# Kernel tuning notes

Measured on AMD Instinct MI355X. Metric: run time of the kernel, lower is better.

Reference implementation:

```python
import jax, jax.numpy as jnp
import numpy as np

N = 100000  # nodes per type (user, tweet)
E = 500000  # edges per relation
D = 128     # input feature dim
H = 128     # hidden dim


def _seg_mean(h_src, src, dst, n_dst):
    # DGL copy_u + mean: mean of source features over incoming edges; zero for in-degree 0.
    msg = h_src[src]                                                    # [E, F] gather
    s = jax.ops.segment_sum(msg, dst, num_segments=n_dst)               # [n_dst, F] scatter-add
    cnt = jax.ops.segment_sum(jnp.ones((src.shape[0], 1), h_src.dtype), dst, num_segments=n_dst)
    return s / jnp.maximum(cnt, 1.0)


def setup_inputs() -> dict:
    key = jax.random.key(0)
    ks = jax.random.split(key, 24)
    f = lambda i, shp, s=1.0: jax.random.normal(ks[i], shp, dtype=jnp.float32) * s
    return {
        'x_user': f(0, (N, D)), 'x_tweet': f(1, (N, D)),
        # layer 1, relation 'posts' (user -> tweet) and 'posted_by' (tweet -> user)
        'w1ps': f(2, (H, D), 0.05), 'b1ps': f(3, (H,), 0.05),
        'w1pn': f(4, (H, D), 0.05), 'b1pn': f(5, (H,), 0.05),
        'w1bs': f(6, (H, D), 0.05), 'b1bs': f(7, (H,), 0.05),
        'w1bn': f(8, (H, D), 0.05), 'b1bn': f(9, (H,), 0.05),
        # layer 2 (out_feats = 1, no activation)
        'w2ps': f(10, (1, H), 0.05), 'b2ps': f(11, (1,), 0.05),
        'w2pn': f(12, (1, H), 0.05), 'b2pn': f(13, (1,), 0.05),
        'w2bs': f(14, (1, H), 0.05), 'b2bs': f(15, (1,), 0.05),
        'w2bn': f(16, (1, H), 0.05), 'b2bn': f(17, (1,), 0.05),
        'src_posts': jax.random.randint(ks[18], (E,), 0, N),
        'dst_posts': jax.random.randint(ks[19], (E,), 0, N),
        'src_pb': jax.random.randint(ks[20], (E,), 0, N),
        'dst_pb': jax.random.randint(ks[21], (E,), 0, N),
    }


def reference(x_user, x_tweet,
              w1ps, b1ps, w1pn, b1pn, w1bs, b1bs, w1bn, b1bn,
              w2ps, b2ps, w2pn, b2pn, w2bs, b2bs, w2bn, b2bn,
              src_posts, dst_posts, src_pb, dst_pb):
    # ---- conv1: DivFeatConv per relation, relu, cross-relation sum (one rel per dst type) ----
    neigh_t = _seg_mean(x_user, src_posts, dst_posts, N)               # user -posts-> tweet
    h_tweet = jax.nn.relu(x_tweet @ w1ps.T + b1ps + neigh_t @ w1pn.T + b1pn)
    neigh_u = _seg_mean(x_tweet, src_pb, dst_pb, N)                    # tweet -posted_by-> user
    h_user = jax.nn.relu(x_user @ w1bs.T + b1bs + neigh_u @ w1bn.T + b1bn)
    # ---- conv2: out_feats=1, identity activation ----
    neigh_t2 = _seg_mean(h_user, src_posts, dst_posts, N)
    out_tweet = h_tweet @ w2ps.T + b2ps + neigh_t2 @ w2pn.T + b2pn     # [N, 1]
    neigh_u2 = _seg_mean(h_tweet, src_pb, dst_pb, N)
    out_user = h_user @ w2bs.T + b2bs + neigh_u2 @ w2bn.T + b2bn       # [N, 1]
    return (out_user, out_tweet)
```

## Files before the change

kernel.cpp:

```cpp
#include <hip/hip_runtime.h>

#define N_NODES 100000
#define N_EDGES 500000
#define DIM 128
#define HSTR 4

typedef __attribute__((ext_vector_type(8))) short short8;
typedef __attribute__((ext_vector_type(4))) float f32x4;

__device__ __forceinline__ ushort f2bf(float f) {
    unsigned u = __float_as_uint(f);
    u += 0x7FFF + ((u >> 16) & 1);
    return (ushort)(u >> 16);
}
__device__ __forceinline__ float bf2f(ushort s) {
    return __uint_as_float(((unsigned)s) << 16);
}


__global__ __launch_bounds__(256) void build_lists2_kernel(
    const int* __restrict__ s0, const int* __restrict__ d0,
    const int* __restrict__ s1, const int* __restrict__ d1,
    int* __restrict__ head2, int2* __restrict__ entry2) {
    const int rel = blockIdx.y;
    const int* src = rel ? s1 : s0;
    const int* dst = rel ? d1 : d0;
    int* head = head2 + (size_t)rel * N_NODES * HSTR;
    int2* entry = entry2 + (size_t)rel * N_EDGES;
    int e = blockIdx.x * 256 + threadIdx.x;
    if (e < N_EDGES) {
        int d = dst[e];
        int old = atomicExch(&head[(size_t)d * HSTR], e);
        entry[e] = make_int2(src[e], old);
    }
}


__global__ __launch_bounds__(256) void cvtw_kernel(
    const float* __restrict__ w0, const float* __restrict__ w1,
    const float* __restrict__ w2, const float* __restrict__ w3,
    ushort* __restrict__ o0, ushort* __restrict__ o1,
    ushort* __restrict__ o2, ushort* __restrict__ o3) {
    int a = blockIdx.y;
    const float* in = (a == 0) ? w0 : (a == 1) ? w1 : (a == 2) ? w2 : w3;
    ushort* out = (a == 0) ? o0 : (a == 1) ? o1 : (a == 2) ? o2 : o3;
    int i = (blockIdx.x * 256 + threadIdx.x) * 4;
    float4 v = *reinterpret_cast<const float4*>(&in[i]);
    ushort4 u = make_ushort4(f2bf(v.x), f2bf(v.y), f2bf(v.z), f2bf(v.w));
    *reinterpret_cast<ushort4*>(&out[i]) = u;
}

__global__ __launch_bounds__(256) void cvtx_kernel(const float* __restrict__ x0,
                                                   const float* __restrict__ x1,
                                                   ushort* __restrict__ o0,
                                                   ushort* __restrict__ o1) {
    const float* in = blockIdx.y ? x1 : x0;
    ushort* out = blockIdx.y ? o1 : o0;
    int i = (blockIdx.x * 256 + threadIdx.x) * 4;
    float4 v = *reinterpret_cast<const float4*>(&in[i]);
    ushort4 u = make_ushort4(f2bf(v.x), f2bf(v.y), f2bf(v.z), f2bf(v.w));
    *reinterpret_cast<ushort4*>(&out[i]) = u;
}


__global__ __launch_bounds__(256) void seg_mean_bf16_list_kernel(
    const ushort* __restrict__ x, const int* __restrict__ head,
    const int2* __restrict__ entry, ushort* __restrict__ outbf) {
    int idx = blockIdx.x * 256 + threadIdx.x;
    int node = idx >> 4;
    if (node >= N_NODES) return;
    int f = (idx & 15) << 3;
    float acc[8];
#pragma unroll
    for (int j = 0; j < 8; ++j) acc[j] = 0.f;
    int cnt = 0;
    int e = head[(size_t)node * HSTR];
    while (e >= 0) {
        int2 nd = entry[e];
        ++cnt;
        short8 v = *reinterpret_cast<const short8*>(&x[(size_t)nd.x * DIM + f]);
#pragma unroll
        for (int j = 0; j < 8; ++j) acc[j] += bf2f((ushort)v[j]);
        e = nd.y;
    }
    float r = 1.0f / fmaxf((float)cnt, 1.0f);
    union { ushort s[8]; uint4 v; } u;
#pragma unroll
    for (int j = 0; j < 8; ++j) u.s[j] = f2bf(acc[j] * r);
    *reinterpret_cast<uint4*>(&outbf[(size_t)node * DIM + f]) = u.v;
}

__global__ __launch_bounds__(256) void seg_mean_f32_list_kernel(
    const float* __restrict__ x, const int* __restrict__ head,
    const int2* __restrict__ entry, ushort* __restrict__ outbf) {
    int idx = blockIdx.x * 256 + threadIdx.x;
    int node = idx >> 5;
    if (node >= N_NODES) return;
    int f = (idx & 31) << 2;
    float4 acc = make_float4(0.f, 0.f, 0.f, 0.f);
    int cnt = 0;
    int e = head[(size_t)node * HSTR];
    while (e >= 0) {
        int2 nd = entry[e];
        ++cnt;
        float4 v = *reinterpret_cast<const float4*>(&x[(size_t)nd.x * DIM + f]);
        acc.x += v.x; acc.y += v.y; acc.z += v.z; acc.w += v.w;
        e = nd.y;
    }
    float r = 1.0f / fmaxf((float)cnt, 1.0f);
    ushort4 u = make_ushort4(f2bf(acc.x * r), f2bf(acc.y * r),
                             f2bf(acc.z * r), f2bf(acc.w * r));
    *reinterpret_cast<ushort4*>(&outbf[node * DIM + f]) = u;
}

__global__ __launch_bounds__(256) void gemm_mfma_bf_kernel(
    const ushort* __restrict__ Xsbf,
    const ushort* __restrict__ Nm,
    const ushort* __restrict__ Wsbf,
    const ushort* __restrict__ Wnbf,
    const float* __restrict__ bs, const float* __restrict__ bn,
    const float* __restrict__ w2a, const float* __restrict__ w2b,
    float* __restrict__ dself, float* __restrict__ dcross) {
    __shared__ ushort sA[128 * 64];
    __shared__ ushort sB[128 * 64];
    __shared__ float pS[2][2][128];

    const int tid = threadIdx.x;
    const int lane = tid & 63;
    const int wid = tid >> 6;
    const int wr = wid >> 1, wc = wid & 1;
    const int lr = lane & 15, lg = lane >> 4;
    const int row0 = blockIdx.x * 128;

    f32x4 acc[4][4];
#pragma unroll
    for (int i = 0; i < 4; ++i)
#pragma unroll
        for (int j = 0; j < 4; ++j) acc[i][j] = (f32x4){0.f, 0.f, 0.f, 0.f};

    const int r = tid >> 1;
    const int hh = tid & 1;
    const int grow = row0 + r;
    const int swzr = (r & 7) << 4;

    for (int kb = 0; kb < 256; kb += 64) {
        const int kg = kb & 127;
        const bool self = (kb < 128);
        __syncthreads();
        {
            const uint4* g = reinterpret_cast<const uint4*>(self ? Xsbf : Nm);
#pragma unroll
            for (int q = 0; q < 4; ++q) {
                uint4 v = make_uint4(0, 0, 0, 0);
                if (grow < N_NODES)
                    v = g[((size_t)grow * DIM + kg + hh * 32 + q * 8) >> 3];
                int byte = (hh * 64 + q * 16) ^ swzr;
                *reinterpret_cast<uint4*>(&sA[r * 64 + (byte >> 1)]) = v;
            }
        }
        {
            const uint4* g = reinterpret_cast<const uint4*>(self ? Wsbf : Wnbf);
#pragma unroll
            for (int q = 0; q < 4; ++q) {
                uint4 v = g[(r * DIM + kg + hh * 32 + q * 8) >> 3];
                int byte = (hh * 64 + q * 16) ^ swzr;
                *reinterpret_cast<uint4*>(&sB[r * 64 + (byte >> 1)]) = v;
            }
        }
        __syncthreads();
#pragma unroll
        for (int ks = 0; ks < 2; ++ks) {
            short8 a[4], b[4];
#pragma unroll
            for (int fm = 0; fm < 4; ++fm) {
                int rr = wr * 64 + fm * 16 + lr;
                int byte = (ks * 64 + lg * 16) ^ ((rr & 7) << 4);
                a[fm] = *reinterpret_cast<const short8*>(&sA[rr * 64 + (byte >> 1)]);
            }
#pragma unroll
            for (int fn = 0; fn < 4; ++fn) {
                int cc = wc * 64 + fn * 16 + lr;
                int byte = (ks * 64 + lg * 16) ^ ((cc & 7) << 4);
                b[fn] = *reinterpret_cast<const short8*>(&sB[cc * 64 + (byte >> 1)]);
            }
#pragma unroll
            for (int fm = 0; fm < 4; ++fm)
#pragma unroll
                for (int fn = 0; fn < 4; ++fn)
                    acc[fm][fn] = __builtin_amdgcn_mfma_f32_16x16x32_bf16(
                        a[fm], b[fn], acc[fm][fn], 0, 0, 0);
        }
    }

    float bias[4], wa[4], wb[4];
#pragma unroll
    for (int fn = 0; fn < 4; ++fn) {
        int c = wc * 64 + fn * 16 + lr;
        bias[fn] = bs[c] + bn[c];
        wa[fn] = w2a[c];
        wb[fn] = w2b[c];
    }
#pragma unroll
    for (int fm = 0; fm < 4; ++fm) {
#pragma unroll
        for (int reg = 0; reg < 4; ++reg) {
            float pa = 0.f, pb = 0.f;
#pragma unroll
            for (int fn = 0; fn < 4; ++fn) {
                float h = fmaxf(acc[fm][fn][reg] + bias[fn], 0.f);
                pa = fmaf(h, wa[fn], pa);
                pb = fmaf(h, wb[fn], pb);
            }
#pragma unroll
            for (int m = 1; m < 16; m <<= 1) {
                pa += __shfl_xor(pa, m);
                pb += __shfl_xor(pb, m);
            }
            if (lr == 0) {
                int rloc = wr * 64 + fm * 16 + lg * 4 + reg;
                pS[wc][0][rloc] = pa;
                pS[wc][1][rloc] = pb;
            }
        }
    }
    __syncthreads();
    if (tid < 128) {
        int go = row0 + tid;
        if (go < N_NODES) {
            dself[go] = pS[0][0][tid] + pS[1][0][tid];
            dcross[go] = pS[0][1][tid] + pS[1][1][tid];
        }
    }
}

__global__ __launch_bounds__(256) void gemm_mfma_kernel(
    const float* __restrict__ Xs, const ushort* __restrict__ Nm,
    const ushort* __restrict__ Wsbf, const ushort* __restrict__ Wnbf,
    const float* __restrict__ bs, const float* __restrict__ bn,
    const float* __restrict__ w2a, const float* __restrict__ w2b,
    float* __restrict__ dself, float* __restrict__ dcross) {
    __shared__ ushort sA[128 * 64];
    __shared__ ushort sB[128 * 64];
    __shared__ float pS[2][2][128];

    const int tid = threadIdx.x;
    const int lane = tid & 63;
    const int wid = tid >> 6;
    const int wr = wid >> 1, wc = wid & 1;
    const int lr = lane & 15, lg = lane >> 4;
    const int row0 = blockIdx.x * 128;

    f32x4 acc[4][4];
#pragma unroll
    for (int i = 0; i < 4; ++i)
#pragma unroll
        for (int j = 0; j < 4; ++j) acc[i][j] = (f32x4){0.f, 0.f, 0.f, 0.f};

    const int r = tid >> 1;
    const int hh = tid & 1;
    const int grow = row0 + r;
    const int swzr = (r & 7) << 4;

    for (int kb = 0; kb < 256; kb += 64) {
        const int kg = kb & 127;
        const bool self = (kb < 128);
        __syncthreads();
        if (self) {
            const float4* g = reinterpret_cast<const float4*>(Xs);
#pragma unroll
            for (int q = 0; q < 4; ++q) {
                float4 v0 = make_float4(0.f, 0.f, 0.f, 0.f), v1 = v0;
                if (grow < N_NODES) {
                    size_t bi = ((size_t)grow * DIM + kg + hh * 32 + q * 8) >> 2;
                    v0 = g[bi];
                    v1 = g[bi + 1];
                }
                union { ushort s[8]; uint4 v; } u;
                u.s[0] = f2bf(v0.x); u.s[1] = f2bf(v0.y);
                u.s[2] = f2bf(v0.z); u.s[3] = f2bf(v0.w);
                u.s[4] = f2bf(v1.x); u.s[5] = f2bf(v1.y);
                u.s[6] = f2bf(v1.z); u.s[7] = f2bf(v1.w);
                int byte = (hh * 64 + q * 16) ^ swzr;
                *reinterpret_cast<uint4*>(&sA[r * 64 + (byte >> 1)]) = u.v;
            }
        } else {
            const uint4* g = reinterpret_cast<const uint4*>(Nm);
#pragma unroll
            for (int q = 0; q < 4; ++q) {
                uint4 v = make_uint4(0, 0, 0, 0);
                if (grow < N_NODES)
                    v = g[((size_t)grow * DIM + kg + hh * 32 + q * 8) >> 3];
                int byte = (hh * 64 + q * 16) ^ swzr;
                *reinterpret_cast<uint4*>(&sA[r * 64 + (byte >> 1)]) = v;
            }
        }
        {
            const uint4* g = reinterpret_cast<const uint4*>(self ? Wsbf : Wnbf);
#pragma unroll
            for (int q = 0; q < 4; ++q) {
                uint4 v = g[(r * DIM + kg + hh * 32 + q * 8) >> 3];
                int byte = (hh * 64 + q * 16) ^ swzr;
                *reinterpret_cast<uint4*>(&sB[r * 64 + (byte >> 1)]) = v;
            }
        }
        __syncthreads();
#pragma unroll
        for (int ks = 0; ks < 2; ++ks) {
            short8 a[4], b[4];
#pragma unroll
            for (int fm = 0; fm < 4; ++fm) {
                int rr = wr * 64 + fm * 16 + lr;
                int byte = (ks * 64 + lg * 16) ^ ((rr & 7) << 4);
                a[fm] = *reinterpret_cast<const short8*>(&sA[rr * 64 + (byte >> 1)]);
            }
#pragma unroll
            for (int fn = 0; fn < 4; ++fn) {
                int cc = wc * 64 + fn * 16 + lr;
                int byte = (ks * 64 + lg * 16) ^ ((cc & 7) << 4);
                b[fn] = *reinterpret_cast<const short8*>(&sB[cc * 64 + (byte >> 1)]);
            }
#pragma unroll
            for (int fm = 0; fm < 4; ++fm)
#pragma unroll
                for (int fn = 0; fn < 4; ++fn)
                    acc[fm][fn] = __builtin_amdgcn_mfma_f32_16x16x32_bf16(
                        a[fm], b[fn], acc[fm][fn], 0, 0, 0);
        }
    }

    float bias[4], wa[4], wb[4];
#pragma unroll
    for (int fn = 0; fn < 4; ++fn) {
        int c = wc * 64 + fn * 16 + lr;
        bias[fn] = bs[c] + bn[c];
        wa[fn] = w2a[c];
        wb[fn] = w2b[c];
    }
#pragma unroll
    for (int fm = 0; fm < 4; ++fm) {
#pragma unroll
        for (int reg = 0; reg < 4; ++reg) {
            float pa = 0.f, pb = 0.f;
#pragma unroll
            for (int fn = 0; fn < 4; ++fn) {
                float h = fmaxf(acc[fm][fn][reg] + bias[fn], 0.f);
                pa = fmaf(h, wa[fn], pa);
                pb = fmaf(h, wb[fn], pb);
            }
#pragma unroll
            for (int m = 1; m < 16; m <<= 1) {
                pa += __shfl_xor(pa, m);
                pb += __shfl_xor(pb, m);
            }
            if (lr == 0) {
                int rloc = wr * 64 + fm * 16 + lg * 4 + reg;
                pS[wc][0][rloc] = pa;
                pS[wc][1][rloc] = pb;
            }
        }
    }
    __syncthreads();
    if (tid < 128) {
        int go = row0 + tid;
        if (go < N_NODES) {
            dself[go] = pS[0][0][tid] + pS[1][0][tid];
            dcross[go] = pS[0][1][tid] + pS[1][1][tid];
        }
    }
}

__global__ __launch_bounds__(256) void scalar_finalize_kernel(
    const float* __restrict__ dself_u, const float* __restrict__ dself_t,
    const float* __restrict__ scross_u, const float* __restrict__ scross_t,
    const int* __restrict__ head2, const int2* __restrict__ entry2,
    const float* __restrict__ b2bs, const float* __restrict__ b2bn,
    const float* __restrict__ b2ps, const float* __restrict__ b2pn,
    float* __restrict__ out) {
    int i = blockIdx.x * 256 + threadIdx.x;
    if (i >= N_NODES) return;
    {
        float a = 0.f; int cnt = 0;
        int e = head2[(size_t)i * HSTR];
        while (e >= 0) {
            int2 nd = entry2[e];
            ++cnt;
            a += scross_u[nd.x];
            e = nd.y;
        }
        out[N_NODES + i] = dself_t[i] + a / fmaxf((float)cnt, 1.0f) + b2ps[0] + b2pn[0];
    }
    {
        float a = 0.f; int cnt = 0;
        int e = head2[((size_t)N_NODES + i) * HSTR];
        while (e >= 0) {
            int2 nd = entry2[(size_t)N_EDGES + e];
            ++cnt;
            a += scross_t[nd.x];
            e = nd.y;
        }
        out[i] = dself_u[i] + a / fmaxf((float)cnt, 1.0f) + b2bs[0] + b2bn[0];
    }
}

extern "C" void kernel_launch(void* const* d_in, const int* in_sizes, int n_in,
                              void* d_out, int out_size, void* d_ws, size_t ws_size,
                              hipStream_t stream) {
    const float* x_user  = (const float*)d_in[0];
    const float* x_tweet = (const float*)d_in[1];
    const float* w1ps = (const float*)d_in[2];  const float* b1ps = (const float*)d_in[3];
    const float* w1pn = (const float*)d_in[4];  const float* b1pn = (const float*)d_in[5];
    const float* w1bs = (const float*)d_in[6];  const float* b1bs = (const float*)d_in[7];
    const float* w1bn = (const float*)d_in[8];  const float* b1bn = (const float*)d_in[9];
    const float* w2ps = (const float*)d_in[10]; const float* b2ps = (const float*)d_in[11];
    const float* w2pn = (const float*)d_in[12]; const float* b2pn = (const float*)d_in[13];
    const float* w2bs = (const float*)d_in[14]; const float* b2bs = (const float*)d_in[15];
    const float* w2bn = (const float*)d_in[16]; const float* b2bn = (const float*)d_in[17];
    const int* src_posts = (const int*)d_in[18];
    const int* dst_posts = (const int*)d_in[19];
    const int* src_pb    = (const int*)d_in[20];
    const int* dst_pb    = (const int*)d_in[21];
    float* out = (float*)d_out;

    char* wsb = (char*)d_ws;
    ushort* nbf     = (ushort*)wsb;   wsb += (size_t)N_NODES * DIM * 2;
    int* head2      = (int*)wsb;      wsb += (size_t)2 * N_NODES * HSTR * 4;
    int2* entry2    = (int2*)wsb;     wsb += (size_t)2 * N_EDGES * 8;
    ushort* wbf_ps  = (ushort*)wsb;   wsb += (size_t)DIM * DIM * 2;
    ushort* wbf_pn  = (ushort*)wsb;   wsb += (size_t)DIM * DIM * 2;
    ushort* wbf_bs  = (ushort*)wsb;   wsb += (size_t)DIM * DIM * 2;
    ushort* wbf_bn  = (ushort*)wsb;   wsb += (size_t)DIM * DIM * 2;
    float* dself_t  = (float*)wsb;    wsb += (size_t)N_NODES * 4;
    float* scross_t = (float*)wsb;    wsb += (size_t)N_NODES * 4;
    float* dself_u  = (float*)wsb;    wsb += (size_t)N_NODES * 4;
    float* scross_u = (float*)wsb;    wsb += (size_t)N_NODES * 4;
    ushort* xbf_u   = (ushort*)wsb;   wsb += (size_t)N_NODES * DIM * 2;
    ushort* xbf_t   = (ushort*)wsb;   wsb += (size_t)N_NODES * DIM * 2;
    const bool use_bf = ((size_t)(wsb - (char*)d_ws) <= ws_size);

    const int* head_posts = head2;
    const int* head_pb    = head2 + (size_t)N_NODES * HSTR;
    const int2* ent_posts = entry2;
    const int2* ent_pb    = entry2 + N_EDGES;

    const int gE = (N_EDGES + 255) / 256;
    const int gN = (N_NODES + 255) / 256;
    const int gG = (N_NODES + 127) / 128;

    cvtw_kernel<<<dim3(16, 4), 256, 0, stream>>>(w1ps, w1pn, w1bs, w1bn,
                                                 wbf_ps, wbf_pn, wbf_bs, wbf_bn);
    if (use_bf)
        cvtx_kernel<<<dim3(12500, 2), 256, 0, stream>>>(x_user, x_tweet, xbf_u, xbf_t);

    hipMemsetAsync(head2, 0xFF, (size_t)2 * N_NODES * HSTR * sizeof(int), stream);
    build_lists2_kernel<<<dim3(gE, 2), 256, 0, stream>>>(src_posts, dst_posts,
                                                         src_pb, dst_pb, head2, entry2);

    if (use_bf) {
        seg_mean_bf16_list_kernel<<<(N_NODES * 16 + 255) / 256, 256, 0, stream>>>(
            xbf_u, head_posts, ent_posts, nbf);
        gemm_mfma_bf_kernel<<<gG, 256, 0, stream>>>(xbf_t, nbf, wbf_ps, wbf_pn,
                                                    b1ps, b1pn, w2ps, w2bn,
                                                    dself_t, scross_t);
    } else {
        seg_mean_f32_list_kernel<<<(N_NODES * 32 + 255) / 256, 256, 0, stream>>>(
            x_user, head_posts, ent_posts, nbf);
        gemm_mfma_kernel<<<gG, 256, 0, stream>>>(x_tweet, nbf, wbf_ps, wbf_pn,
                                                 b1ps, b1pn, w2ps, w2bn,
                                                 dself_t, scross_t);
    }

    if (use_bf) {
        seg_mean_bf16_list_kernel<<<(N_NODES * 16 + 255) / 256, 256, 0, stream>>>(
            xbf_t, head_pb, ent_pb, nbf);
        gemm_mfma_bf_kernel<<<gG, 256, 0, stream>>>(xbf_u, nbf, wbf_bs, wbf_bn,
                                                    b1bs, b1bn, w2bs, w2pn,
                                                    dself_u, scross_u);
    } else {
        seg_mean_f32_list_kernel<<<(N_NODES * 32 + 255) / 256, 256, 0, stream>>>(
            x_tweet, head_pb, ent_pb, nbf);
        gemm_mfma_kernel<<<gG, 256, 0, stream>>>(x_user, nbf, wbf_bs, wbf_bn,
                                                 b1bs, b1bn, w2bs, w2pn,
                                                 dself_u, scross_u);
    }

    scalar_finalize_kernel<<<gN, 256, 0, stream>>>(dself_u, dself_t, scross_u, scross_t,
                                                   head2, entry2, b2bs, b2bn, b2ps, b2pn,
                                                   out);
}
```

Baseline: 211.4 us.

## Merge independent stages into multi-role fat kernels and compact head array

Independent stages are packed into shared launches that branch on block index: list building plus weight and feature conversion run as one kernel, the second segment-mean runs alongside the first GEMM, and one scalar mean runs alongside the second GEMM, leaving a smaller tail kernel. The per-node head array loses its stride-4 padding, so it takes less memory and needs a smaller memset. The goal is fewer launches and gaps between them, with latency-bound gather work overlapping compute-bound GEMM blocks. In exchange, blocks with very different resource use share one kernel, so occupancy is set by the heaviest role (GEMM shared memory), and removing the padding could raise atomic contention on adjacent head entries.

```diff
diff --git a/kernel.cpp b/kernel.cpp
--- a/kernel.cpp
+++ b/kernel.cpp
@@ -3,7 +3,11 @@
 #define N_NODES 100000
 #define N_EDGES 500000
 #define DIM 128
-#define HSTR 4
+#define GB_E 1954
+#define GB_N 391
+#define GB_CVT 12500
+#define GB_G 782
+#define GB_SEG 6250
 
 typedef __attribute__((ext_vector_type(8))) short short8;
 typedef __attribute__((ext_vector_type(4))) float f32x4;
@@ -18,21 +22,269 @@
 }
 
 
-__global__ __launch_bounds__(256) void build_lists2_kernel(
-    const int* __restrict__ s0, const int* __restrict__ d0,
-    const int* __restrict__ s1, const int* __restrict__ d1,
-    int* __restrict__ head2, int2* __restrict__ entry2) {
-    const int rel = blockIdx.y;
-    const int* src = rel ? s1 : s0;
-    const int* dst = rel ? d1 : d0;
-    int* head = head2 + (size_t)rel * N_NODES * HSTR;
-    int2* entry = entry2 + (size_t)rel * N_EDGES;
-    int e = blockIdx.x * 256 + threadIdx.x;
+__device__ __forceinline__ void build_body(const int* __restrict__ src,
+                                           const int* __restrict__ dst,
+                                           int* __restrict__ head,
+                                           int2* __restrict__ entry, int bid) {
+    int e = bid * 256 + threadIdx.x;
     if (e < N_EDGES) {
         int d = dst[e];
-        int old = atomicExch(&head[(size_t)d * HSTR], e);
+        int old = atomicExch(&head[d], e);
         entry[e] = make_int2(src[e], old);
     }
+}
+
+__device__ __forceinline__ void cvt_body(const float* __restrict__ in,
+                                         ushort* __restrict__ out, int bid) {
+    int i = (bid * 256 + threadIdx.x) * 4;
+    float4 v = *reinterpret_cast<const float4*>(&in[i]);
+    ushort4 u = make_ushort4(f2bf(v.x), f2bf(v.y), f2bf(v.z), f2bf(v.w));
+    *reinterpret_cast<ushort4*>(&out[i]) = u;
+}
+
+__device__ __forceinline__ void seg_body(const ushort* __restrict__ x,
+                                         const int* __restrict__ head,
+                                         const int2* __restrict__ entry,
+                                         ushort* __restrict__ outbf, int bid) {
+    int idx = bid * 256 + threadIdx.x;
+    int node = idx >> 4;
+    if (node >= N_NODES) return;
+    int f = (idx & 15) << 3;
+    float acc[8];
+#pragma unroll
+    for (int j = 0; j < 8; ++j) acc[j] = 0.f;
+    int cnt = 0;
+    int e = head[node];
+    while (e >= 0) {
+        int2 nd = entry[e];
+        ++cnt;
+        short8 v = *reinterpret_cast<const short8*>(&x[(size_t)nd.x * DIM + f]);
+#pragma unroll
+        for (int j = 0; j < 8; ++j) acc[j] += bf2f((ushort)v[j]);
+        e = nd.y;
+    }
+    float r = 1.0f / fmaxf((float)cnt, 1.0f);
+    union { ushort s[8]; uint4 v; } u;
+#pragma unroll
+    for (int j = 0; j < 8; ++j) u.s[j] = f2bf(acc[j] * r);
+    *reinterpret_cast<uint4*>(&outbf[(size_t)node * DIM + f]) = u.v;
+}
+
+__device__ __forceinline__ float smean_body(const float* __restrict__ sval,
+                                            const int* __restrict__ head,
+                                            const int2* __restrict__ entry, int node) {
+    float a = 0.f;
+    int cnt = 0;
+    int e = head[node];
+    while (e >= 0) {
+        int2 nd = entry[e];
+        ++cnt;
+        a += sval[nd.x];
+        e = nd.y;
+    }
+    return a / fmaxf((float)cnt, 1.0f);
+}
+
+__device__ __forceinline__ void gemm_body(
+    const ushort* __restrict__ Xsbf, const ushort* __restrict__ Nm,
+    const ushort* __restrict__ Wsbf, const ushort* __restrict__ Wnbf,
+    const float* __restrict__ bs, const float* __restrict__ bn,
+    const float* __restrict__ w2a, const float* __restrict__ w2b,
+    float* __restrict__ dself, float* __restrict__ dcross, int blk) {
+    __shared__ ushort sA[128 * 64];
+    __shared__ ushort sB[128 * 64];
+    __shared__ float pS[2][2][128];
+
+    const int tid = threadIdx.x;
+    const int lane = tid & 63;
+    const int wid = tid >> 6;
+    const int wr = wid >> 1, wc = wid & 1;
+    const int lr = lane & 15, lg = lane >> 4;
+    const int row0 = blk * 128;
+
+    f32x4 acc[4][4];
+#pragma unroll
+    for (int i = 0; i < 4; ++i)
+#pragma unroll
+        for (int j = 0; j < 4; ++j) acc[i][j] = (f32x4){0.f, 0.f, 0.f, 0.f};
+
+    const int r = tid >> 1;
+    const int hh = tid & 1;
+    const int grow = row0 + r;
+    const int swzr = (r & 7) << 4;
+
+    for (int kb = 0; kb < 256; kb += 64) {
+        const int kg = kb & 127;
+        const bool self = (kb < 128);
+        __syncthreads();
+        {
+            const uint4* g = reinterpret_cast<const uint4*>(self ? Xsbf : Nm);
+#pragma unroll
+            for (int q = 0; q < 4; ++q) {
+                uint4 v = make_uint4(0, 0, 0, 0);
+                if (grow < N_NODES)
+                    v = g[((size_t)grow * DIM + kg + hh * 32 + q * 8) >> 3];
+                int byte = (hh * 64 + q * 16) ^ swzr;
+                *reinterpret_cast<uint4*>(&sA[r * 64 + (byte >> 1)]) = v;
+            }
+        }
+        {
+            const uint4* g = reinterpret_cast<const uint4*>(self ? Wsbf : Wnbf);
+#pragma unroll
+            for (int q = 0; q < 4; ++q) {
+                uint4 v = g[(r * DIM + kg + hh * 32 + q * 8) >> 3];
+                int byte = (hh * 64 + q * 16) ^ swzr;
+                *reinterpret_cast<uint4*>(&sB[r * 64 + (byte >> 1)]) = v;
+            }
+        }
+        __syncthreads();
+#pragma unroll
+        for (int ks = 0; ks < 2; ++ks) {
+            short8 a[4], b[4];
+#pragma unroll
+            for (int fm = 0; fm < 4; ++fm) {
+                int rr = wr * 64 + fm * 16 + lr;
+                int byte = (ks * 64 + lg * 16) ^ ((rr & 7) << 4);
+                a[fm] = *reinterpret_cast<const short8*>(&sA[rr * 64 + (byte >> 1)]);
+            }
+#pragma unroll
+            for (int fn = 0; fn < 4; ++fn) {
+                int cc = wc * 64 + fn * 16 + lr;
+                int byte = (ks * 64 + lg * 16) ^ ((cc & 7) << 4);
+                b[fn] = *reinterpret_cast<const short8*>(&sB[cc * 64 + (byte >> 1)]);
+            }
+#pragma unroll
+            for (int fm = 0; fm < 4; ++fm)
+#pragma unroll
+                for (int fn = 0; fn < 4; ++fn)
+                    acc[fm][fn] = __builtin_amdgcn_mfma_f32_16x16x32_bf16(
+                        a[fm], b[fn], acc[fm][fn], 0, 0, 0);
+        }
+    }
+
+    float bias[4], wa[4], wb[4];
+#pragma unroll
+    for (int fn = 0; fn < 4; ++fn) {
+        int c = wc * 64 + fn * 16 + lr;
+        bias[fn] = bs[c] + bn[c];
+        wa[fn] = w2a[c];
+        wb[fn] = w2b[c];
+    }
+#pragma unroll
+    for (int fm = 0; fm < 4; ++fm) {
+#pragma unroll
+        for (int reg = 0; reg < 4; ++reg) {
+            float pa = 0.f, pb = 0.f;
+#pragma unroll
+            for (int fn = 0; fn < 4; ++fn) {
+                float h = fmaxf(acc[fm][fn][reg] + bias[fn], 0.f);
+                pa = fmaf(h, wa[fn], pa);
+                pb = fmaf(h, wb[fn], pb);
+            }
+#pragma unroll
+            for (int m = 1; m < 16; m <<= 1) {
+                pa += __shfl_xor(pa, m);
+                pb += __shfl_xor(pb, m);
+            }
+            if (lr == 0) {
+                int rloc = wr * 64 + fm * 16 + lg * 4 + reg;
+                pS[wc][0][rloc] = pa;
+                pS[wc][1][rloc] = pb;
+            }
+        }
+    }
+    __syncthreads();
+    if (tid < 128) {
+        int go = row0 + tid;
+        if (go < N_NODES) {
+            dself[go] = pS[0][0][tid] + pS[1][0][tid];
+            dcross[go] = pS[0][1][tid] + pS[1][1][tid];
+        }
+    }
+}
+
+
+__global__ __launch_bounds__(256) void fatA_kernel(
+    const int* __restrict__ sp, const int* __restrict__ dp,
+    const int* __restrict__ sb, const int* __restrict__ db,
+    int* __restrict__ head2, int2* __restrict__ entry2,
+    const float* __restrict__ w0, const float* __restrict__ w1,
+    const float* __restrict__ w2, const float* __restrict__ w3,
+    ushort* __restrict__ o0, ushort* __restrict__ o1,
+    ushort* __restrict__ o2, ushort* __restrict__ o3,
+    const float* __restrict__ xu, const float* __restrict__ xt,
+    ushort* __restrict__ xbf_u, ushort* __restrict__ xbf_t) {
+    int bid = blockIdx.x;
+    if (bid < 2 * GB_E) {
+        int rel = (bid >= GB_E);
+        build_body(rel ? sb : sp, rel ? db : dp, head2 + (size_t)rel * N_NODES,
+                   entry2 + (size_t)rel * N_EDGES, bid - rel * GB_E);
+    } else if (bid < 2 * GB_E + 64) {
+        int b = bid - 2 * GB_E;
+        int a = b >> 4;
+        const float* in = (a == 0) ? w0 : (a == 1) ? w1 : (a == 2) ? w2 : w3;
+        ushort* out = (a == 0) ? o0 : (a == 1) ? o1 : (a == 2) ? o2 : o3;
+        cvt_body(in, out, b & 15);
+    } else {
+        int b = bid - 2 * GB_E - 64;
+        int which = (b >= GB_CVT);
+        cvt_body(which ? xt : xu, which ? xbf_t : xbf_u, b - which * GB_CVT);
+    }
+}
+
+__global__ __launch_bounds__(256) void seg_only_kernel(
+    const ushort* __restrict__ x, const int* __restrict__ head,
+    const int2* __restrict__ entry, ushort* __restrict__ outbf) {
+    seg_body(x, head, entry, outbf, blockIdx.x);
+}
+
+__global__ __launch_bounds__(256) void fatB_kernel(
+    const ushort* __restrict__ xbf_t, const ushort* __restrict__ nbf0,
+    const ushort* __restrict__ wbf_ps, const ushort* __restrict__ wbf_pn,
+    const float* __restrict__ b1ps, const float* __restrict__ b1pn,
+    const float* __restrict__ w2ps, const float* __restrict__ w2bn,
+    float* __restrict__ dself_t, float* __restrict__ scross_t,
+    const int* __restrict__ head_pb, const int2* __restrict__ ent_pb,
+    ushort* __restrict__ nbf1) {
+    int bid = blockIdx.x;
+    if (bid < GB_G)
+        gemm_body(xbf_t, nbf0, wbf_ps, wbf_pn, b1ps, b1pn, w2ps, w2bn,
+                  dself_t, scross_t, bid);
+    else
+        seg_body(xbf_t, head_pb, ent_pb, nbf1, bid - GB_G);
+}
+
+__global__ __launch_bounds__(256) void fatC_kernel(
+    const ushort* __restrict__ xbf_u, const ushort* __restrict__ nbf1,
+    const ushort* __restrict__ wbf_bs, const ushort* __restrict__ wbf_bn,
+    const float* __restrict__ b1bs, const float* __restrict__ b1bn,
+    const float* __restrict__ w2bs, const float* __restrict__ w2pn,
+    float* __restrict__ dself_u, float* __restrict__ scross_u,
+    const float* __restrict__ scross_t,
+    const int* __restrict__ head_pb, const int2* __restrict__ ent_pb,
+    float* __restrict__ smean_u) {
+    int bid = blockIdx.x;
+    if (bid < GB_G) {
+        gemm_body(xbf_u, nbf1, wbf_bs, wbf_bn, b1bs, b1bn, w2bs, w2pn,
+                  dself_u, scross_u, bid);
+    } else {
+        int i = (bid - GB_G) * 256 + threadIdx.x;
+        if (i < N_NODES) smean_u[i] = smean_body(scross_t, head_pb, ent_pb, i);
+    }
+}
+
+__global__ __launch_bounds__(256) void tail_kernel(
+    const float* __restrict__ dself_u, const float* __restrict__ smean_u,
+    const float* __restrict__ dself_t, const float* __restrict__ scross_u,
+    const int* __restrict__ head_posts, const int2* __restrict__ ent_posts,
+    const float* __restrict__ b2bs, const float* __restrict__ b2bn,
+    const float* __restrict__ b2ps, const float* __restrict__ b2pn,
+    float* __restrict__ out) {
+    int i = blockIdx.x * 256 + threadIdx.x;
+    if (i >= N_NODES) return;
+    out[N_NODES + i] = dself_t[i] + smean_body(scross_u, head_posts, ent_posts, i)
+                       + b2ps[0] + b2pn[0];
+    out[i] = dself_u[i] + smean_u[i] + b2bs[0] + b2bn[0];
 }
 
 
@@ -44,50 +296,16 @@
     int a = blockIdx.y;
     const float* in = (a == 0) ? w0 : (a == 1) ? w1 : (a == 2) ? w2 : w3;
     ushort* out = (a == 0) ? o0 : (a == 1) ? o1 : (a == 2) ? o2 : o3;
-    int i = (blockIdx.x * 256 + threadIdx.x) * 4;
-    float4 v = *reinterpret_cast<const float4*>(&in[i]);
-    ushort4 u = make_ushort4(f2bf(v.x), f2bf(v.y), f2bf(v.z), f2bf(v.w));
-    *reinterpret_cast<ushort4*>(&out[i]) = u;
-}
-
-__global__ __launch_bounds__(256) void cvtx_kernel(const float* __restrict__ x0,
-                                                   const float* __restrict__ x1,
-                                                   ushort* __restrict__ o0,
-                                                   ushort* __restrict__ o1) {
-    const float* in = blockIdx.y ? x1 : x0;
-    ushort* out = blockIdx.y ? o1 : o0;
-    int i = (blockIdx.x * 256 + threadIdx.x) * 4;
-    float4 v = *reinterpret_cast<const float4*>(&in[i]);
-    ushort4 u = make_ushort4(f2bf(v.x), f2bf(v.y), f2bf(v.z), f2bf(v.w));
-    *reinterpret_cast<ushort4*>(&out[i]) = u;
-}
-
-
-__global__ __launch_bounds__(256) void seg_mean_bf16_list_kernel(
-    const ushort* __restrict__ x, const int* __restrict__ head,
-    const int2* __restrict__ entry, ushort* __restrict__ outbf) {
-    int idx = blockIdx.x * 256 + threadIdx.x;
-    int node = idx >> 4;
-    if (node >= N_NODES) return;
-    int f = (idx & 15) << 3;
-    float acc[8];
-#pragma unroll
-    for (int j = 0; j < 8; ++j) acc[j] = 0.f;
-    int cnt = 0;
-    int e = head[(size_t)node * HSTR];
-    while (e >= 0) {
-        int2 nd = entry[e];
-        ++cnt;
-        short8 v = *reinterpret_cast<const short8*>(&x[(size_t)nd.x * DIM + f]);
-#pragma unroll
-        for (int j = 0; j < 8; ++j) acc[j] += bf2f((ushort)v[j]);
-        e = nd.y;
-    }
-    float r = 1.0f / fmaxf((float)cnt, 1.0f);
-    union { ushort s[8]; uint4 v; } u;
-#pragma unroll
-    for (int j = 0; j < 8; ++j) u.s[j] = f2bf(acc[j] * r);
-    *reinterpret_cast<uint4*>(&outbf[(size_t)node * DIM + f]) = u.v;
+    cvt_body(in, out, blockIdx.x);
+}
+
+__global__ __launch_bounds__(256) void build_lists2_kernel(
+    const int* __restrict__ s0, const int* __restrict__ d0,
+    const int* __restrict__ s1, const int* __restrict__ d1,
+    int* __restrict__ head2, int2* __restrict__ entry2) {
+    const int rel = blockIdx.y;
+    build_body(rel ? s1 : s0, rel ? d1 : d0, head2 + (size_t)rel * N_NODES,
+               entry2 + (size_t)rel * N_EDGES, blockIdx.x);
 }
 
 __global__ __launch_bounds__(256) void seg_mean_f32_list_kernel(
@@ -99,7 +317,7 @@
     int f = (idx & 31) << 2;
     float4 acc = make_float4(0.f, 0.f, 0.f, 0.f);
     int cnt = 0;
-    int e = head[(size_t)node * HSTR];
+    int e = head[node];
     while (e >= 0) {
         int2 nd = entry[e];
         ++cnt;
@@ -113,127 +331,7 @@
     *reinterpret_cast<ushort4*>(&outbf[node * DIM + f]) = u;
 }
 
-__global__ __launch_bounds__(256) void gemm_mfma_bf_kernel(
-    const ushort* __restrict__ Xsbf,
-    const ushort* __restrict__ Nm,
-    const ushort* __restrict__ Wsbf,
-    const ushort* __restrict__ Wnbf,
-    const float* __restrict__ bs, const float* __restrict__ bn,
-    const float* __restrict__ w2a, const float* __restrict__ w2b,
-    float* __restrict__ dself, float* __restrict__ dcross) {
-    __shared__ ushort sA[128 * 64];
-    __shared__ ushort sB[128 * 64];
-    __shared__ float pS[2][2][128];
-
-    const int tid = threadIdx.x;
-    const int lane = tid & 63;
-    const int wid = tid >> 6;
-    const int wr = wid >> 1, wc = wid & 1;
-    const int lr = lane & 15, lg = lane >> 4;
-    const int row0 = blockIdx.x * 128;
-
-    f32x4 acc[4][4];
-#pragma unroll
-    for (int i = 0; i < 4; ++i)
-#pragma unroll
-        for (int j = 0; j < 4; ++j) acc[i][j] = (f32x4){0.f, 0.f, 0.f, 0.f};
-
-    const int r = tid >> 1;
-    const int hh = tid & 1;
-    const int grow = row0 + r;
-    const int swzr = (r & 7) << 4;
-
-    for (int kb = 0; kb < 256; kb += 64) {
-        const int kg = kb & 127;
-        const bool self = (kb < 128);
-        __syncthreads();
-        {
-            const uint4* g = reinterpret_cast<const uint4*>(self ? Xsbf : Nm);
-#pragma unroll
-            for (int q = 0; q < 4; ++q) {
-                uint4 v = make_uint4(0, 0, 0, 0);
-                if (grow < N_NODES)
-                    v = g[((size_t)grow * DIM + kg + hh * 32 + q * 8) >> 3];
-                int byte = (hh * 64 + q * 16) ^ swzr;
-                *reinterpret_cast<uint4*>(&sA[r * 64 + (byte >> 1)]) = v;
-            }
-        }
-        {
-            const uint4* g = reinterpret_cast<const uint4*>(self ? Wsbf : Wnbf);
-#pragma unroll
-            for (int q = 0; q < 4; ++q) {
-                uint4 v = g[(r * DIM + kg + hh * 32 + q * 8) >> 3];
-                int byte = (hh * 64 + q * 16) ^ swzr;
-                *reinterpret_cast<uint4*>(&sB[r * 64 + (byte >> 1)]) = v;
-            }
-        }
-        __syncthreads();
-#pragma unroll
-        for (int ks = 0; ks < 2; ++ks) {
-            short8 a[4], b[4];
-#pragma unroll
-            for (int fm = 0; fm < 4; ++fm) {
-                int rr = wr * 64 + fm * 16 + lr;
-                int byte = (ks * 64 + lg * 16) ^ ((rr & 7) << 4);
-                a[fm] = *reinterpret_cast<const short8*>(&sA[rr * 64 + (byte >> 1)]);
-            }
-#pragma unroll
-            for (int fn = 0; fn < 4; ++fn) {
-                int cc = wc * 64 + fn * 16 + lr;
-                int byte = (ks * 64 + lg * 16) ^ ((cc & 7) << 4);
-                b[fn] = *reinterpret_cast<const short8*>(&sB[cc * 64 + (byte >> 1)]);
-            }
-#pragma unroll
-            for (int fm = 0; fm < 4; ++fm)
-#pragma unroll
-                for (int fn = 0; fn < 4; ++fn)
-                    acc[fm][fn] = __builtin_amdgcn_mfma_f32_16x16x32_bf16(
-                        a[fm], b[fn], acc[fm][fn], 0, 0, 0);
-        }
-    }
-
-    float bias[4], wa[4], wb[4];
-#pragma unroll
-    for (int fn = 0; fn < 4; ++fn) {
-        int c = wc * 64 + fn * 16 + lr;
-        bias[fn] = bs[c] + bn[c];
-        wa[fn] = w2a[c];
-        wb[fn] = w2b[c];
-    }
-#pragma unroll
-    for (int fm = 0; fm < 4; ++fm) {
-#pragma unroll
-        for (int reg = 0; reg < 4; ++reg) {
-            float pa = 0.f, pb = 0.f;
-#pragma unroll
-            for (int fn = 0; fn < 4; ++fn) {
-                float h = fmaxf(acc[fm][fn][reg] + bias[fn], 0.f);
-                pa = fmaf(h, wa[fn], pa);
-                pb = fmaf(h, wb[fn], pb);
-            }
-#pragma unroll
-            for (int m = 1; m < 16; m <<= 1) {
-                pa += __shfl_xor(pa, m);
-                pb += __shfl_xor(pb, m);
-            }
-            if (lr == 0) {
-                int rloc = wr * 64 + fm * 16 + lg * 4 + reg;
-                pS[wc][0][rloc] = pa;
-                pS[wc][1][rloc] = pb;
-            }
-        }
-    }
-    __syncthreads();
-    if (tid < 128) {
-        int go = row0 + tid;
-        if (go < N_NODES) {
-            dself[go] = pS[0][0][tid] + pS[1][0][tid];
-            dcross[go] = pS[0][1][tid] + pS[1][1][tid];
-        }
-    }
-}
-
-__global__ __launch_bounds__(256) void gemm_mfma_kernel(
+__global__ __launch_bounds__(256) void gemm_mfma_f32_kernel(
     const float* __restrict__ Xs, const ushort* __restrict__ Nm,
     const ushort* __restrict__ Wsbf, const ushort* __restrict__ Wnbf,
     const float* __restrict__ bs, const float* __restrict__ bn,
@@ -378,29 +476,12 @@
     float* __restrict__ out) {
     int i = blockIdx.x * 256 + threadIdx.x;
     if (i >= N_NODES) return;
-    {
-        float a = 0.f; int cnt = 0;
-        int e = head2[(size_t)i * HSTR];
-        while (e >= 0) {
-            int2 nd = entry2[e];
-            ++cnt;
-            a += scross_u[nd.x];
-            e = nd.y;
-        }
-        out[N_NODES + i] = dself_t[i] + a / fmaxf((float)cnt, 1.0f) + b2ps[0] + b2pn[0];
-    }
-    {
-        float a = 0.f; int cnt = 0;
-        int e = head2[((size_t)N_NODES + i) * HSTR];
-        while (e >= 0) {
-            int2 nd = entry2[(size_t)N_EDGES + e];
-            ++cnt;
-            a += scross_t[nd.x];
-            e = nd.y;
-        }
-        out[i] = dself_u[i] + a / fmaxf((float)cnt, 1.0f) + b2bs[0] + b2bn[0];
-    }
-}
+    out[N_NODES + i] = dself_t[i] + smean_body(scross_u, head2, entry2, i)
+                       + b2ps[0] + b2pn[0];
+    out[i] = dself_u[i] + smean_body(scross_t, head2 + N_NODES, entry2 + N_EDGES, i)
+             + b2bs[0] + b2bn[0];
+}
+
 
 extern "C" void kernel_launch(void* const* d_in, const int* in_sizes, int n_in,
                               void* d_out, int out_size, void* d_ws, size_t ws_size,
@@ -422,8 +503,8 @@
     float* out = (float*)d_out;
 
     char* wsb = (char*)d_ws;
-    ushort* nbf     = (ushort*)wsb;   wsb += (size_t)N_NODES * DIM * 2;
-    int* head2      = (int*)wsb;      wsb += (size_t)2 * N_NODES * HSTR * 4;
+    ushort* nbf0    = (ushort*)wsb;   wsb += (size_t)N_NODES * DIM * 2;
+    int* head2      = (int*)wsb;      wsb += (size_t)2 * N_NODES * 4;
     int2* entry2    = (int2*)wsb;     wsb += (size_t)2 * N_EDGES * 8;
     ushort* wbf_ps  = (ushort*)wsb;   wsb += (size_t)DIM * DIM * 2;
     ushort* wbf_pn  = (ushort*)wsb;   wsb += (size_t)DIM * DIM * 2;
@@ -433,57 +514,57 @@
     float* scross_t = (float*)wsb;    wsb += (size_t)N_NODES * 4;
     float* dself_u  = (float*)wsb;    wsb += (size_t)N_NODES * 4;
     float* scross_u = (float*)wsb;    wsb += (size_t)N_NODES * 4;
+    float* smean_u  = (float*)wsb;    wsb += (size_t)N_NODES * 4;
+    ushort* nbf1    = (ushort*)wsb;   wsb += (size_t)N_NODES * DIM * 2;
     ushort* xbf_u   = (ushort*)wsb;   wsb += (size_t)N_NODES * DIM * 2;
     ushort* xbf_t   = (ushort*)wsb;   wsb += (size_t)N_NODES * DIM * 2;
     const bool use_bf = ((size_t)(wsb - (char*)d_ws) <= ws_size);
 
     const int* head_posts = head2;
-    const int* head_pb    = head2 + (size_t)N_NODES * HSTR;
+    const int* head_pb    = head2 + N_NODES;
     const int2* ent_posts = entry2;
     const int2* ent_pb    = entry2 + N_EDGES;
 
-    const int gE = (N_EDGES + 255) / 256;
-    const int gN = (N_NODES + 255) / 256;
-    const int gG = (N_NODES + 127) / 128;
-
-    cvtw_kernel<<<dim3(16, 4), 256, 0, stream>>>(w1ps, w1pn, w1bs, w1bn,
-                                                 wbf_ps, wbf_pn, wbf_bs, wbf_bn);
-    if (use_bf)
-        cvtx_kernel<<<dim3(12500, 2), 256, 0, stream>>>(x_user, x_tweet, xbf_u, xbf_t);
-
-    hipMemsetAsync(head2, 0xFF, (size_t)2 * N_NODES * HSTR * sizeof(int), stream);
-    build_lists2_kernel<<<dim3(gE, 2), 256, 0, stream>>>(src_posts, dst_posts,
-                                                         src_pb, dst_pb, head2, entry2);
-
-    if (use_bf) {
-        seg_mean_bf16_list_kernel<<<(N_NODES * 16 + 255) / 256, 256, 0, stream>>>(
-            xbf_u, head_posts, ent_posts, nbf);
-        gemm_mfma_bf_kernel<<<gG, 256, 0, stream>>>(xbf_t, nbf, wbf_ps, wbf_pn,
-                                                    b1ps, b1pn, w2ps, w2bn,
-                                                    dself_t, scross_t);
-    } else {
+    hipMemsetAsync(head2, 0xFF, (size_t)2 * N_NODES * sizeof(int), stream);
+
+    if (!use_bf) {
+        cvtw_kernel<<<dim3(16, 4), 256, 0, stream>>>(w1ps, w1pn, w1bs, w1bn,
+                                                     wbf_ps, wbf_pn, wbf_bs, wbf_bn);
+        build_lists2_kernel<<<dim3(GB_E, 2), 256, 0, stream>>>(
+            src_posts, dst_posts, src_pb, dst_pb, head2, entry2);
         seg_mean_f32_list_kernel<<<(N_NODES * 32 + 255) / 256, 256, 0, stream>>>(
-            x_user, head_posts, ent_posts, nbf);
-        gemm_mfma_kernel<<<gG, 256, 0, stream>>>(x_tweet, nbf, wbf_ps, wbf_pn,
-                                                 b1ps, b1pn, w2ps, w2bn,
-                                                 dself_t, scross_t);
-    }
-
-    if (use_bf) {
-        seg_mean_bf16_list_kernel<<<(N_NODES * 16 + 255) / 256, 256, 0, stream>>>(
-            xbf_t, head_pb, ent_pb, nbf);
-        gemm_mfma_bf_kernel<<<gG, 256, 0, stream>>>(xbf_u, nbf, wbf_bs, wbf_bn,
-                                                    b1bs, b1bn, w2bs, w2pn,
-                                                    dself_u, scross_u);
-    } else {
+            x_user, head_posts, ent_posts, nbf0);
+        gemm_mfma_f32_kernel<<<GB_G, 256, 0, stream>>>(x_tweet, nbf0, wbf_ps, wbf_pn,
+                                                       b1ps, b1pn, w2ps, w2bn,
+                                                       dself_t, scross_t);
         seg_mean_f32_list_kernel<<<(N_NODES * 32 + 255) / 256, 256, 0, stream>>>(
-            x_tweet, head_pb, ent_pb, nbf);
-        gemm_mfma_kernel<<<gG, 256, 0, stream>>>(x_user, nbf, wbf_bs, wbf_bn,
-                                                 b1bs, b1bn, w2bs, w2pn,
-                                                 dself_u, scross_u);
-    }
-
-    scalar_finalize_kernel<<<gN, 256, 0, stream>>>(dself_u, dself_t, scross_u, scross_t,
-                                                   head2, entry2, b2bs, b2bn, b2ps, b2pn,
-                                                   out);
-}
+            x_tweet, head_pb, ent_pb, nbf0);
+        gemm_mfma_f32_kernel<<<GB_G, 256, 0, stream>>>(x_user, nbf0, wbf_bs, wbf_bn,
+                                                       b1bs, b1bn, w2bs, w2pn,
+                                                       dself_u, scross_u);
+        scalar_finalize_kernel<<<GB_N, 256, 0, stream>>>(dself_u, dself_t,
+                                                         scross_u, scross_t,
+                                                         head2, entry2,
+                                                         b2bs, b2bn, b2ps, b2pn, out);
+        return;
+    }
+
+    fatA_kernel<<<2 * GB_E + 64 + 2 * GB_CVT, 256, 0, stream>>>(
+        src_posts, dst_posts, src_pb, dst_pb, head2, entry2,
+        w1ps, w1pn, w1bs, w1bn, wbf_ps, wbf_pn, wbf_bs, wbf_bn,
+        x_user, x_tweet, xbf_u, xbf_t);
+
+    seg_only_kernel<<<GB_SEG, 256, 0, stream>>>(xbf_u, head_posts, ent_posts, nbf0);
+
+    fatB_kernel<<<GB_G + GB_SEG, 256, 0, stream>>>(
+        xbf_t, nbf0, wbf_ps, wbf_pn, b1ps, b1pn, w2ps, w2bn,
+        dself_t, scross_t, head_pb, ent_pb, nbf1);
+
+    fatC_kernel<<<GB_G + GB_N, 256, 0, stream>>>(
+        xbf_u, nbf1, wbf_bs, wbf_bn, b1bs, b1bn, w2bs, w2pn,
+        dself_u, scross_u, scross_t, head_pb, ent_pb, smean_u);
+
+    tail_kernel<<<GB_N, 256, 0, stream>>>(dself_u, smean_u, dself_t, scross_u,
+                                          head_posts, ent_posts,
+                                          b2bs, b2bn, b2ps, b2pn, out);
+}
```

Result: slower. 221.4 us (+4.8%).
